# Kernel optimization log

Measured on AMD Instinct MI355X. Metric: run time of the kernel, lower is better.

The kernel has to match this reference:

```python
import jax, jax.numpy as jnp
import numpy as np

VOCAB, EDIM, ENC, H, OUT = 50000, 128, 128, 100, 104
B, L, NPT = 128, 64, 64          # batch, statements per seq, nodes per statement tree
N = B * L * NPT                  # 524288 total nodes
MAXD = 6                         # max depth of a 64-node complete binary tree


def setup_inputs() -> dict:
    key = jax.random.key(0)
    ks = jax.random.split(key, 14)
    tokens = jax.random.randint(ks[0], (N,), 0, VOCAB)
    # structured tree topology: each statement tree is a 64-node complete binary tree
    local = np.arange(NPT)
    par_local = np.where(local == 0, 0, (local - 1) // 2)
    depth_local = np.floor(np.log2(local + 1)).astype(np.int32)
    base = np.repeat(np.arange(B * L) * NPT, NPT)
    parent = jnp.asarray(base + np.tile(par_local, B * L), dtype=jnp.int32)
    depth = jnp.asarray(np.tile(depth_local, B * L), dtype=jnp.int32)
    tree_id = jnp.asarray(np.repeat(np.arange(B * L), NPT), dtype=jnp.int32)
    nrm = lambda k, s, sc: jax.random.normal(k, s, jnp.float32) * sc
    return {
        "tokens": tokens, "parent": parent, "depth": depth, "tree_id": tree_id,
        "emb": nrm(ks[1], (VOCAB, EDIM), 0.02),
        "W_lin": nrm(ks[2], (ENC, EDIM), 0.05), "b_lin": nrm(ks[3], (ENC,), 0.05),
        "Wi_f": nrm(ks[4], (3 * H, ENC), 0.05), "Wh_f": nrm(ks[5], (3 * H, H), 0.05),
        "bi_f": nrm(ks[6], (3 * H,), 0.05), "bh_f": nrm(ks[7], (3 * H,), 0.05),
        "Wi_b": nrm(ks[8], (3 * H, ENC), 0.05), "Wh_b": nrm(ks[9], (3 * H, H), 0.05),
        "bi_b": nrm(ks[10], (3 * H,), 0.05), "bh_b": nrm(ks[11], (3 * H,), 0.05),
        "W_fc": nrm(ks[12], (OUT, 2 * H), 0.05), "b_fc": nrm(ks[13], (OUT,), 0.05),
    }


def _gru_scan(x_seq, Wi, Wh, bi, bh):
    # x_seq: [L, B, ENC] -> outputs [L, B, H]. Matches torch.nn.GRU cell math.
    def step(hprev, xt):
        gi = xt @ Wi.T + bi              # [B, 3H]
        gh = hprev @ Wh.T + bh
        ir, iz, inn = jnp.split(gi, 3, axis=-1)
        hr, hz, hn = jnp.split(gh, 3, axis=-1)
        r = jax.nn.sigmoid(ir + hr)
        z = jax.nn.sigmoid(iz + hz)
        n = jnp.tanh(inn + r * hn)
        hnew = (1.0 - z) * n + z * hprev
        return hnew, hnew
    h0 = jnp.zeros((x_seq.shape[1], Wh.shape[1]), x_seq.dtype)
    _, ys = jax.lax.scan(step, h0, x_seq)
    return ys


def reference(tokens, parent, depth, tree_id, emb, W_lin, b_lin,
              Wi_f, Wh_f, bi_f, bh_f, Wi_b, Wh_b, bi_b, bh_b, W_fc, b_fc):
    # per-node value: linear(embedding(token))   [N, ENC]
    h = emb[tokens] @ W_lin.T + b_lin
    # bottom-up subtree sum: h(node) = v(node) + sum(h(children)), batched by depth level
    for d in range(MAXD, 0, -1):
        contrib = jnp.where((depth == d)[:, None], h, 0.0)
        h = h.at[parent].add(contrib)
    # TreeEncoder output: max over all node hidden states of each tree
    encodes = jax.ops.segment_max(h, tree_id, num_segments=B * L)  # [B*L, ENC]
    x = encodes.reshape(B, L, ENC).transpose(1, 0, 2)              # [L, B, ENC]
    yf = _gru_scan(x, Wi_f, Wh_f, bi_f, bh_f)                      # [L, B, H]
    yb = _gru_scan(x[::-1], Wi_b, Wh_b, bi_b, bh_b)[::-1]
    gru_out = jnp.concatenate([yf, yb], axis=-1)                   # [L, B, 2H]
    pooled = gru_out.max(axis=0)                                   # [B, 2H]
    return pooled @ W_fc.T + b_fc                                  # [B, OUT]
```

## Files before the change

kernel.cpp:

```cpp
#include <hip/hip_runtime.h>
#include <hip/hip_bf16.h>

typedef __bf16 bf16_t;
typedef __attribute__((ext_vector_type(8))) __bf16 bf16x8;
typedef __attribute__((ext_vector_type(4))) float f32x4;

#define TREES 8192
#define ENC 128
#define HH 100
#define G3 300
#define GSTRIDE 304
#define BB 128
#define LL 64
#define OUTD 104
#define TPB_TREES 8

__device__ __forceinline__ float sigm(float x) { return 1.0f / (1.0f + __expf(-x)); }
__device__ __forceinline__ float tanh_f(float x) { return 2.0f / (1.0f + __expf(-2.0f * x)) - 1.0f; }
__device__ __forceinline__ float bflo(unsigned int u) { return __builtin_bit_cast(float, u << 16); }
__device__ __forceinline__ float bfhi(unsigned int u) { return __builtin_bit_cast(float, u & 0xffff0000u); }

__device__ __forceinline__ void ldsbar() {
  asm volatile("s_waitcnt lgkmcnt(0)\n\ts_barrier" ::: "memory");
}

__device__ __forceinline__ int subtree_size(int n) {
  int np1 = n + 1;
  int d = 31 - __clz(np1);
  return ((64 >> d) - 1) + (((np1 & (np1 - 1)) == 0) ? 1 : 0);
}

__global__ __launch_bounds__(256) void k0_prep(const float* __restrict__ W_lin,
                                               const float* __restrict__ Wi_f,
                                               const float* __restrict__ Wi_b,
                                               const float* __restrict__ emb,
                                               bf16_t* __restrict__ Wbf,
                                               bf16_t* __restrict__ Wibf,
                                               bf16_t* __restrict__ embbf) {
  int i = blockIdx.x * 256 + threadIdx.x;
#pragma unroll
  for (int r = 0; r < 4; ++r) {
    int e = i + r * 524288;
    if (e < 1600000) {
      float4 v = ((const float4*)emb)[e];
      ushort4 u;
      u.x = __builtin_bit_cast(unsigned short, (bf16_t)v.x);
      u.y = __builtin_bit_cast(unsigned short, (bf16_t)v.y);
      u.z = __builtin_bit_cast(unsigned short, (bf16_t)v.z);
      u.w = __builtin_bit_cast(unsigned short, (bf16_t)v.w);
      ((ushort4*)embbf)[e] = u;
    }
  }
  if (i < 128 * 128) Wbf[i] = (bf16_t)W_lin[i];
  if (i < 608 * 128) {
    int jg = i >> 7, k = i & 127;
    int dir = (jg >= GSTRIDE) ? 1 : 0;
    int j = jg - dir * GSTRIDE;
    float v = 0.0f;
    if (j < G3) v = dir ? Wi_b[j * 128 + k] : Wi_f[j * 128 + k];
    Wibf[i] = (bf16_t)v;
  }
}

__global__ __launch_bounds__(256) void k1_tree(const int* __restrict__ tokens,
                                               const bf16_t* __restrict__ embbf,
                                               const bf16_t* __restrict__ Wbf,
                                               const float* __restrict__ b_lin,
                                               float* __restrict__ encodes) {
  __shared__ float s_[64][129];
  __shared__ float maxbuf[2][128];
  __shared__ float sb[128];
  int tid = threadIdx.x;
  int wave = tid >> 6;
  int lane = tid & 63;
  int ri = lane & 15;
  int kg = lane >> 4;
  int wm = wave >> 1;
  int wn = wave & 1;

  if (tid < 128) sb[tid] = b_lin[tid];

  bf16x8 bfr[4][4];
#pragma unroll
  for (int ks = 0; ks < 4; ++ks)
#pragma unroll
    for (int ni = 0; ni < 4; ++ni)
      bfr[ks][ni] = *(const bf16x8*)(Wbf + (size_t)((wn * 4 + ni) * 16 + ri) * 128 +
                                     ks * 32 + kg * 8);

  float szs[2][4];
#pragma unroll
  for (int mi = 0; mi < 2; ++mi)
#pragma unroll
    for (int rr = 0; rr < 4; ++rr)
      szs[mi][rr] = (float)subtree_size(wm * 32 + mi * 16 + kg * 4 + rr);

  int n = tid >> 2;
  int q = tid & 3;
  int c = tid >> 1;
  int half = tid & 1;
  int pc = (c & ~31) | ((((c >> 3) + (c >> 5)) & 3) << 3) | (c & 7);
  int tree0 = blockIdx.x * TPB_TREES;

  uint4 pre[4];
  {
    int tok = tokens[tree0 * 64 + n];
    const uint4* src = (const uint4*)(embbf + (size_t)tok * ENC) + q * 4;
#pragma unroll
    for (int i = 0; i < 4; ++i) pre[i] = src[i];
  }
  __syncthreads();

  for (int t = 0; t < TPB_TREES; ++t) {
    int tree = tree0 + t;

#pragma unroll
    for (int i = 0; i < 4; ++i) {
      uint4 p = pre[i];
      float4 f0 = {bflo(p.x), bfhi(p.x), bflo(p.y), bfhi(p.y)};
      float4 f1 = {bflo(p.z), bfhi(p.z), bflo(p.w), bfhi(p.w)};
      int col = q * 32 + (((i + q) & 3) << 3);
      *(float4*)&s_[n][col] = f0;
      *(float4*)&s_[n][col + 4] = f1;
    }

    if (t + 1 < TPB_TREES) {
      int tok = tokens[(tree + 1) * 64 + n];
      const uint4* src = (const uint4*)(embbf + (size_t)tok * ENC) + q * 4;
#pragma unroll
      for (int i = 0; i < 4; ++i) pre[i] = src[i];
    }
    ldsbar();

    if (half == 0) s_[31][pc] += s_[63][pc];
    {
      float r[8];
      int pb = 15 + half * 8;
#pragma unroll
      for (int i = 0; i < 8; ++i) {
        int p = pb + i;
        r[i] = s_[p][pc] + s_[2 * p + 1][pc] + s_[2 * p + 2][pc];
        s_[p][pc] = r[i];
      }
      float tt[4];
      int pb2 = 7 + half * 4;
#pragma unroll
      for (int i = 0; i < 4; ++i) {
        int p = pb2 + i;
        tt[i] = s_[p][pc] + r[2 * i] + r[2 * i + 1];
        s_[p][pc] = tt[i];
      }
      float uu[2];
      int pb3 = 3 + half * 2;
#pragma unroll
      for (int i = 0; i < 2; ++i) {
        int p = pb3 + i;
        uu[i] = s_[p][pc] + tt[2 * i] + tt[2 * i + 1];
        s_[p][pc] = uu[i];
      }
      int p1 = 1 + half;
      float w1 = s_[p1][pc] + uu[0] + uu[1];
      s_[p1][pc] = w1;
      float w2 = __shfl_xor(w1, 1);
      if (half == 0) s_[0][pc] = s_[0][pc] + w1 + w2;
    }
    ldsbar();

    f32x4 acc[2][4];
#pragma unroll
    for (int mi = 0; mi < 2; ++mi)
#pragma unroll
      for (int ni = 0; ni < 4; ++ni) {
        f32x4 z = {0.f, 0.f, 0.f, 0.f};
        acc[mi][ni] = z;
      }
#pragma unroll
    for (int ks = 0; ks < 4; ++ks) {
      int k0p = ks * 32 + (((kg + ks) & 3) << 3);
#pragma unroll
      for (int mi = 0; mi < 2; ++mi) {
        int row = wm * 32 + mi * 16 + ri;
        float4 a0 = *(const float4*)&s_[row][k0p];
        float4 a1 = *(const float4*)&s_[row][k0p + 4];
        bf16x8 afr;
        afr[0] = (bf16_t)a0.x; afr[1] = (bf16_t)a0.y; afr[2] = (bf16_t)a0.z; afr[3] = (bf16_t)a0.w;
        afr[4] = (bf16_t)a1.x; afr[5] = (bf16_t)a1.y; afr[6] = (bf16_t)a1.z; afr[7] = (bf16_t)a1.w;
#pragma unroll
        for (int ni = 0; ni < 4; ++ni)
          acc[mi][ni] = __builtin_amdgcn_mfma_f32_16x16x32_bf16(afr, bfr[ks][ni], acc[mi][ni], 0, 0, 0);
      }
    }

    float cmax[4];
#pragma unroll
    for (int ni = 0; ni < 4; ++ni) {
      float bl = sb[(wn * 4 + ni) * 16 + ri];
      float m = -1e30f;
#pragma unroll
      for (int mi = 0; mi < 2; ++mi) {
        f32x4 a = acc[mi][ni];
        m = fmaxf(m, fmaxf(fmaxf(a.x + szs[mi][0] * bl, a.y + szs[mi][1] * bl),
                           fmaxf(a.z + szs[mi][2] * bl, a.w + szs[mi][3] * bl)));
      }
      cmax[ni] = m;
    }
#pragma unroll
    for (int off = 16; off < 64; off <<= 1) {
#pragma unroll
      for (int ni = 0; ni < 4; ++ni)
        cmax[ni] = fmaxf(cmax[ni], __shfl_xor(cmax[ni], off));
    }
    if (lane < 16) {
#pragma unroll
      for (int ni = 0; ni < 4; ++ni) maxbuf[wm][(wn * 4 + ni) * 16 + lane] = cmax[ni];
    }
    ldsbar();
    if (tid < 128) {
      encodes[(size_t)tree * ENC + tid] = fmaxf(maxbuf[0][tid], maxbuf[1][tid]);
    }
  }
}

__global__ __launch_bounds__(256) void k2_gi(const float* __restrict__ encodes,
                                             const bf16_t* __restrict__ Wibf,
                                             const float* __restrict__ bi_f,
                                             const float* __restrict__ bi_b,
                                             bf16_t* __restrict__ GIb) {
  int tid = threadIdx.x;
  int wave = tid >> 6;
  int lane = tid & 63;
  int ri = lane & 15;
  int kg = lane >> 4;
  int m0 = blockIdx.x * 16;

  f32x4 acc[10];
#pragma unroll
  for (int i = 0; i < 10; ++i) {
    f32x4 z = {0.f, 0.f, 0.f, 0.f};
    acc[i] = z;
  }

  int r = m0 + ri;
  int er = (r & 127) * 64 + (r >> 7);
  const float* arow = encodes + (size_t)er * ENC;
#pragma unroll
  for (int ks = 0; ks < 4; ++ks) {
    int k0 = ks * 32 + kg * 8;
    float4 a0 = *(const float4*)(arow + k0);
    float4 a1 = *(const float4*)(arow + k0 + 4);
    bf16x8 afr;
    afr[0] = (bf16_t)a0.x; afr[1] = (bf16_t)a0.y; afr[2] = (bf16_t)a0.z; afr[3] = (bf16_t)a0.w;
    afr[4] = (bf16_t)a1.x; afr[5] = (bf16_t)a1.y; afr[6] = (bf16_t)a1.z; afr[7] = (bf16_t)a1.w;
#pragma unroll
    for (int i = 0; i < 10; ++i) {
      int nt = wave + i * 4;
      if (nt < 38) {
        bf16x8 bfr = *(const bf16x8*)(Wibf + (nt * 16 + ri) * 128 + k0);
        acc[i] = __builtin_amdgcn_mfma_f32_16x16x32_bf16(afr, bfr, acc[i], 0, 0, 0);
      }
    }
  }
#pragma unroll
  for (int i = 0; i < 10; ++i) {
    int nt = wave + i * 4;
    if (nt >= 38) continue;
    int jg = nt * 16 + ri;
    int dir = (jg >= GSTRIDE) ? 1 : 0;
    int j = jg - dir * GSTRIDE;
    if (j >= G3) continue;
    float bias = dir ? bi_b[j] : bi_f[j];
#pragma unroll
    for (int rr = 0; rr < 4; ++rr) {
      int rowg = m0 + kg * 4 + rr;
      int l = rowg >> 7, b = rowg & 127;
      GIb[(((size_t)dir * LL + l) * BB + b) * GSTRIDE + j] = (bf16_t)(acc[i][rr] + bias);
    }
  }
}

__global__ __launch_bounds__(640) void k3_gru(const bf16_t* __restrict__ GIb,
                                              const float* __restrict__ Wh_f,
                                              const float* __restrict__ Wh_b,
                                              const float* __restrict__ bh_f,
                                              const float* __restrict__ bh_b,
                                              float* __restrict__ pooled) {
  int blk = blockIdx.x;
  int dir = blk >> 7;
  int b = blk & 127;
  int tid = threadIdx.x;
  __shared__ __align__(16) float h_lds[104];
  __shared__ float gh_lds[304];
  __shared__ float gi_lds[2][304];
  const float* Wh = dir ? Wh_b : Wh_f;
  const float* bh = dir ? bh_b : bh_f;

  int j = tid >> 1;
  int kg = tid & 1;
  int kbase = kg * 52;
  bool isdot = (tid < 600);

  float4 wv[13];
  float bhj = 0.f;
  if (isdot) {
#pragma unroll
    for (int c = 0; c < 13; ++c) {
      int k0 = kbase + c * 4;
      float4 v;
      v.x = (k0 + 0 < HH) ? Wh[j * HH + k0 + 0] : 0.f;
      v.y = (k0 + 1 < HH) ? Wh[j * HH + k0 + 1] : 0.f;
      v.z = (k0 + 2 < HH) ? Wh[j * HH + k0 + 2] : 0.f;
      v.w = (k0 + 3 < HH) ? Wh[j * HH + k0 + 3] : 0.f;
      wv[c] = v;
    }
    if (kg == 0) bhj = bh[j];
  }
  if (tid < 104) h_lds[tid] = 0.f;

  const bf16_t* giB = GIb + (size_t)dir * LL * BB * GSTRIDE + (size_t)b * GSTRIDE;
  if (tid < G3) {
    int la0 = dir ? 63 : 0;
    gi_lds[0][tid] = (float)giB[(size_t)la0 * BB * GSTRIDE + tid];
  }
  float ymax = -1e30f;
  __syncthreads();

  for (int step = 0; step < 64; ++step) {
    int cur = step & 1;
    int nxt = cur ^ 1;
    float ginext = 0.f;
    if (tid < G3) {
      int ns = (step < 63) ? step + 1 : 63;
      int la = dir ? (63 - ns) : ns;
      ginext = (float)giB[(size_t)la * BB * GSTRIDE + tid];
    }
    if (isdot) {
      float a0 = 0.f, a1 = 0.f, a2 = 0.f, a3 = 0.f;
#pragma unroll
      for (int c = 0; c < 13; ++c) {
        float4 hv = *(const float4*)&h_lds[kbase + c * 4];
        a0 += wv[c].x * hv.x;
        a1 += wv[c].y * hv.y;
        a2 += wv[c].z * hv.z;
        a3 += wv[c].w * hv.w;
      }
      float p = (a0 + a1) + (a2 + a3);
      p += __shfl_xor(p, 1);
      if (kg == 0) gh_lds[j] = p + bhj;
    }
    __syncthreads();
    if (tid < HH) {
      float r = sigm(gi_lds[cur][tid] + gh_lds[tid]);
      float z = sigm(gi_lds[cur][100 + tid] + gh_lds[100 + tid]);
      float n = tanh_f(gi_lds[cur][200 + tid] + r * gh_lds[200 + tid]);
      float hnew = (1.f - z) * n + z * h_lds[tid];
      ymax = fmaxf(ymax, hnew);
      h_lds[tid] = hnew;
    }
    if (tid < G3 && step < 63) gi_lds[nxt][tid] = ginext;
    __syncthreads();
  }
  if (tid < HH) pooled[(size_t)b * 200 + dir * 100 + tid] = ymax;
}

__global__ __launch_bounds__(128) void k4_fc(const float* __restrict__ pooled,
                                             const float* __restrict__ W_fc,
                                             const float* __restrict__ b_fc,
                                             float* __restrict__ out) {
  int b = blockIdx.x;
  int o = threadIdx.x;
  if (o >= OUTD) return;
  const float* p = pooled + (size_t)b * 200;
  const float* w = W_fc + (size_t)o * 200;
  float acc = b_fc[o];
#pragma unroll 8
  for (int j = 0; j < 200; ++j) acc += p[j] * w[j];
  out[(size_t)b * OUTD + o] = acc;
}

extern "C" void kernel_launch(void* const* d_in, const int* in_sizes, int n_in,
                              void* d_out, int out_size, void* d_ws, size_t ws_size,
                              hipStream_t stream) {
  const int* tokens = (const int*)d_in[0];
  const float* emb = (const float*)d_in[4];
  const float* W_lin = (const float*)d_in[5];
  const float* b_lin = (const float*)d_in[6];
  const float* Wi_f = (const float*)d_in[7];
  const float* Wh_f = (const float*)d_in[8];
  const float* bi_f = (const float*)d_in[9];
  const float* bh_f = (const float*)d_in[10];
  const float* Wi_b = (const float*)d_in[11];
  const float* Wh_b = (const float*)d_in[12];
  const float* bi_b = (const float*)d_in[13];
  const float* bh_b = (const float*)d_in[14];
  const float* W_fc = (const float*)d_in[15];
  const float* b_fc = (const float*)d_in[16];

  float* encodes = (float*)d_ws;
  float* GIreg = encodes + (size_t)TREES * ENC;
  float* pooled = GIreg + (size_t)2 * LL * BB * GSTRIDE;
  bf16_t* Wbf = (bf16_t*)(pooled + (size_t)BB * 200);
  bf16_t* Wibf = Wbf + 128 * 128;
  bf16_t* embbf = (bf16_t*)GIreg;
  bf16_t* GIb = (bf16_t*)GIreg;

  k0_prep<<<2048, 256, 0, stream>>>(W_lin, Wi_f, Wi_b, emb, Wbf, Wibf, embbf);
  k1_tree<<<TREES / TPB_TREES, 256, 0, stream>>>(tokens, embbf, Wbf, b_lin, encodes);
  k2_gi<<<512, 256, 0, stream>>>(encodes, Wibf, bi_f, bi_b, GIb);
  k3_gru<<<256, 640, 0, stream>>>(GIb, Wh_f, Wh_b, bh_f, bh_b, pooled);
  k4_fc<<<BB, 128, 0, stream>>>(pooled, W_fc, b_fc, (float*)d_out);
}
```

Before: 152.5 us.

## Restructure GRU step to one barrier per step using shuffle-based gate exchange

The GRU recurrence kernel now assigns each hidden unit j an 8-lane group. Six lanes compute the r/z/n recurrent dot-product halves and exchange the partial sums through lane shuffles instead of an LDS gh buffer, so each step needs a single barrier instead of two. The hidden state is double-buffered in LDS, and the input-gate values are prefetched into registers instead of staged in LDS. The block grows from 640 to 832 threads, and two of every eight lanes sit idle. Weight rows are loaded as float4 with a zeroed tail.

```diff
diff --git a/kernel.cpp b/kernel.cpp
--- a/kernel.cpp
+++ b/kernel.cpp
@@ -278,7 +278,7 @@
   }
 }
 
-__global__ __launch_bounds__(640) void k3_gru(const bf16_t* __restrict__ GIb,
+__global__ __launch_bounds__(832) void k3_gru(const bf16_t* __restrict__ GIb,
                                               const float* __restrict__ Wh_f,
                                               const float* __restrict__ Wh_b,
                                               const float* __restrict__ bh_f,
@@ -288,78 +288,77 @@
   int dir = blk >> 7;
   int b = blk & 127;
   int tid = threadIdx.x;
-  __shared__ __align__(16) float h_lds[104];
-  __shared__ float gh_lds[304];
-  __shared__ float gi_lds[2][304];
+  __shared__ __align__(16) float h_lds[2][104];
+  int j = tid >> 3;
+  int sub = tid & 7;
+  int g = sub >> 1;
+  int half = sub & 1;
+  bool isdot = (sub < 6) && (j < HH);
+  bool isgate = (sub == 0) && (j < HH);
   const float* Wh = dir ? Wh_b : Wh_f;
   const float* bh = dir ? bh_b : bh_f;
 
-  int j = tid >> 1;
-  int kg = tid & 1;
-  int kbase = kg * 52;
-  bool isdot = (tid < 600);
-
   float4 wv[13];
-  float bhj = 0.f;
   if (isdot) {
-#pragma unroll
-    for (int c = 0; c < 13; ++c) {
-      int k0 = kbase + c * 4;
-      float4 v;
-      v.x = (k0 + 0 < HH) ? Wh[j * HH + k0 + 0] : 0.f;
-      v.y = (k0 + 1 < HH) ? Wh[j * HH + k0 + 1] : 0.f;
-      v.z = (k0 + 2 < HH) ? Wh[j * HH + k0 + 2] : 0.f;
-      v.w = (k0 + 3 < HH) ? Wh[j * HH + k0 + 3] : 0.f;
-      wv[c] = v;
-    }
-    if (kg == 0) bhj = bh[j];
-  }
-  if (tid < 104) h_lds[tid] = 0.f;
-
-  const bf16_t* giB = GIb + (size_t)dir * LL * BB * GSTRIDE + (size_t)b * GSTRIDE;
-  if (tid < G3) {
+    const float4* wrow = (const float4*)(Wh + (size_t)(g * HH + j) * HH + half * 52);
+#pragma unroll
+    for (int c = 0; c < 13; ++c) wv[c] = wrow[c];
+    if (half) { float4 z = {0.f, 0.f, 0.f, 0.f}; wv[12] = z; }
+  }
+  if (tid < 104) { h_lds[0][tid] = 0.f; h_lds[1][tid] = 0.f; }
+
+  float bhr = 0.f, bhz = 0.f, bhn = 0.f;
+  float gir = 0.f, giz = 0.f, gin = 0.f;
+  const bf16_t* gbase = nullptr;
+  if (isgate) {
+    bhr = bh[j]; bhz = bh[HH + j]; bhn = bh[2 * HH + j];
+    gbase = GIb + (size_t)dir * LL * BB * GSTRIDE + (size_t)b * GSTRIDE + j;
     int la0 = dir ? 63 : 0;
-    gi_lds[0][tid] = (float)giB[(size_t)la0 * BB * GSTRIDE + tid];
-  }
-  float ymax = -1e30f;
+    const bf16_t* p0 = gbase + (size_t)la0 * BB * GSTRIDE;
+    gir = (float)p0[0]; giz = (float)p0[100]; gin = (float)p0[200];
+  }
+  float h_prev = 0.f, ymax = -1e30f;
   __syncthreads();
 
+  int cur = 0;
   for (int step = 0; step < 64; ++step) {
-    int cur = step & 1;
-    int nxt = cur ^ 1;
-    float ginext = 0.f;
-    if (tid < G3) {
-      int ns = (step < 63) ? step + 1 : 63;
-      int la = dir ? (63 - ns) : ns;
-      ginext = (float)giB[(size_t)la * BB * GSTRIDE + tid];
-    }
+    float gnr = 0.f, gnz = 0.f, gnn = 0.f;
+    if (isgate && step < 63) {
+      int la = dir ? (62 - step) : (step + 1);
+      const bf16_t* p = gbase + (size_t)la * BB * GSTRIDE;
+      gnr = (float)p[0]; gnz = (float)p[100]; gnn = (float)p[200];
+    }
+    float p = 0.f;
     if (isdot) {
       float a0 = 0.f, a1 = 0.f, a2 = 0.f, a3 = 0.f;
+      const float* hb = &h_lds[cur][half * 52];
 #pragma unroll
       for (int c = 0; c < 13; ++c) {
-        float4 hv = *(const float4*)&h_lds[kbase + c * 4];
+        float4 hv = *(const float4*)(hb + c * 4);
         a0 += wv[c].x * hv.x;
         a1 += wv[c].y * hv.y;
         a2 += wv[c].z * hv.z;
         a3 += wv[c].w * hv.w;
       }
-      float p = (a0 + a1) + (a2 + a3);
-      p += __shfl_xor(p, 1);
-      if (kg == 0) gh_lds[j] = p + bhj;
-    }
-    __syncthreads();
-    if (tid < HH) {
-      float r = sigm(gi_lds[cur][tid] + gh_lds[tid]);
-      float z = sigm(gi_lds[cur][100 + tid] + gh_lds[100 + tid]);
-      float n = tanh_f(gi_lds[cur][200 + tid] + r * gh_lds[200 + tid]);
-      float hnew = (1.f - z) * n + z * h_lds[tid];
+      p = (a0 + a1) + (a2 + a3);
+    }
+    p += __shfl_xor(p, 1);
+    float gh2 = __shfl_xor(p, 2);
+    float gh4 = __shfl_xor(p, 4);
+    if (isgate) {
+      float r = sigm(gir + p + bhr);
+      float z = sigm(giz + gh2 + bhz);
+      float n = tanh_f(gin + r * (gh4 + bhn));
+      float hnew = (1.f - z) * n + z * h_prev;
       ymax = fmaxf(ymax, hnew);
-      h_lds[tid] = hnew;
-    }
-    if (tid < G3 && step < 63) gi_lds[nxt][tid] = ginext;
-    __syncthreads();
-  }
-  if (tid < HH) pooled[(size_t)b * 200 + dir * 100 + tid] = ymax;
+      h_lds[cur ^ 1][j] = hnew;
+      h_prev = hnew;
+      gir = gnr; giz = gnz; gin = gnn;
+    }
+    ldsbar();
+    cur ^= 1;
+  }
+  if (isgate) pooled[(size_t)b * 200 + dir * HH + j] = ymax;
 }
 
 __global__ __launch_bounds__(128) void k4_fc(const float* __restrict__ pooled,
@@ -406,6 +405,6 @@
   k0_prep<<<2048, 256, 0, stream>>>(W_lin, Wi_f, Wi_b, emb, Wbf, Wibf, embbf);
   k1_tree<<<TREES / TPB_TREES, 256, 0, stream>>>(tokens, embbf, Wbf, b_lin, encodes);
   k2_gi<<<512, 256, 0, stream>>>(encodes, Wibf, bi_f, bi_b, GIb);
-  k3_gru<<<256, 640, 0, stream>>>(GIb, Wh_f, Wh_b, bh_f, bh_b, pooled);
+  k3_gru<<<256, 832, 0, stream>>>(GIb, Wh_f, Wh_b, bh_f, bh_b, pooled);
   k4_fc<<<BB, 128, 0, stream>>>(pooled, W_fc, b_fc, (float*)d_out);
 }
```

New measurement: 187.4 us. 22.9% more time.

## Restructure GRU recurrent matvec to four rows per thread with half the threads

Applied to the files above, without the earlier changes.

The recurrent GRU kernel now runs 320 threads instead of 640. Each thread computes four gate rows over a quarter of the hidden dimension, so every h value read from LDS is reused across four rows, and the partial sums are combined with two xor shuffles. The recurrent biases move into the gate-update threads, and __syncthreads is replaced by an explicit lgkmcnt wait plus barrier. The aim is fewer LDS reads and fewer waves per barrier in this serial, latency-bound loop, at the cost of about 112 weight registers per thread.

```diff
diff --git a/kernel.cpp b/kernel.cpp
--- a/kernel.cpp
+++ b/kernel.cpp
@@ -278,7 +278,7 @@
   }
 }
 
-__global__ __launch_bounds__(640) void k3_gru(const bf16_t* __restrict__ GIb,
+__global__ __launch_bounds__(320) void k3_gru(const bf16_t* __restrict__ GIb,
                                               const float* __restrict__ Wh_f,
                                               const float* __restrict__ Wh_b,
                                               const float* __restrict__ bh_f,
@@ -288,33 +288,39 @@
   int dir = blk >> 7;
   int b = blk & 127;
   int tid = threadIdx.x;
-  __shared__ __align__(16) float h_lds[104];
+  __shared__ __align__(16) float h_lds[112];
   __shared__ float gh_lds[304];
   __shared__ float gi_lds[2][304];
   const float* Wh = dir ? Wh_b : Wh_f;
   const float* bh = dir ? bh_b : bh_f;
 
-  int j = tid >> 1;
-  int kg = tid & 1;
-  int kbase = kg * 52;
-  bool isdot = (tid < 600);
-
-  float4 wv[13];
-  float bhj = 0.f;
-  if (isdot) {
-#pragma unroll
-    for (int c = 0; c < 13; ++c) {
-      int k0 = kbase + c * 4;
-      float4 v;
-      v.x = (k0 + 0 < HH) ? Wh[j * HH + k0 + 0] : 0.f;
-      v.y = (k0 + 1 < HH) ? Wh[j * HH + k0 + 1] : 0.f;
-      v.z = (k0 + 2 < HH) ? Wh[j * HH + k0 + 2] : 0.f;
-      v.w = (k0 + 3 < HH) ? Wh[j * HH + k0 + 3] : 0.f;
-      wv[c] = v;
-    }
-    if (kg == 0) bhj = bh[j];
-  }
-  if (tid < 104) h_lds[tid] = 0.f;
+  int jg = tid >> 2;
+  int ksub = tid & 3;
+  bool isdot = (jg < 75);
+  int koff = (ksub == 0) ? 0 : (4 + ksub * 24);
+  int kn = (ksub == 0) ? 28 : 24;
+
+  float4 wv[4][7];
+#pragma unroll
+  for (int r = 0; r < 4; ++r)
+#pragma unroll
+    for (int c7 = 0; c7 < 7; ++c7) {
+      float4 v = {0.f, 0.f, 0.f, 0.f};
+      if (isdot) {
+        const float* wrow = Wh + (size_t)(jg * 4 + r) * HH + koff;
+        int c0 = c7 * 4;
+        if (c0 + 0 < kn) v.x = wrow[c0 + 0];
+        if (c0 + 1 < kn) v.y = wrow[c0 + 1];
+        if (c0 + 2 < kn) v.z = wrow[c0 + 2];
+        if (c0 + 3 < kn) v.w = wrow[c0 + 3];
+      }
+      wv[r][c7] = v;
+    }
+
+  if (tid < 112) h_lds[tid] = 0.f;
+
+  float bhr = 0.f, bhz = 0.f, bhn = 0.f;
+  if (tid < HH) { bhr = bh[tid]; bhz = bh[HH + tid]; bhn = bh[2 * HH + tid]; }
 
   const bf16_t* giB = GIb + (size_t)dir * LL * BB * GSTRIDE + (size_t)b * GSTRIDE;
   if (tid < G3) {
@@ -324,42 +330,56 @@
   float ymax = -1e30f;
   __syncthreads();
 
+  int cur = 0;
   for (int step = 0; step < 64; ++step) {
-    int cur = step & 1;
     int nxt = cur ^ 1;
     float ginext = 0.f;
-    if (tid < G3) {
-      int ns = (step < 63) ? step + 1 : 63;
-      int la = dir ? (63 - ns) : ns;
+    if (tid < G3 && step < 63) {
+      int la = dir ? (62 - step) : (step + 1);
       ginext = (float)giB[(size_t)la * BB * GSTRIDE + tid];
     }
+    f32x4 facc = {0.f, 0.f, 0.f, 0.f};
     if (isdot) {
+      float4 hv[7];
+#pragma unroll
+      for (int c7 = 0; c7 < 7; ++c7) hv[c7] = *(const float4*)&h_lds[koff + c7 * 4];
       float a0 = 0.f, a1 = 0.f, a2 = 0.f, a3 = 0.f;
 #pragma unroll
-      for (int c = 0; c < 13; ++c) {
-        float4 hv = *(const float4*)&h_lds[kbase + c * 4];
-        a0 += wv[c].x * hv.x;
-        a1 += wv[c].y * hv.y;
-        a2 += wv[c].z * hv.z;
-        a3 += wv[c].w * hv.w;
-      }
-      float p = (a0 + a1) + (a2 + a3);
-      p += __shfl_xor(p, 1);
-      if (kg == 0) gh_lds[j] = p + bhj;
-    }
-    __syncthreads();
+      for (int c7 = 0; c7 < 7; ++c7) {
+        a0 += wv[0][c7].x * hv[c7].x + wv[0][c7].y * hv[c7].y +
+              wv[0][c7].z * hv[c7].z + wv[0][c7].w * hv[c7].w;
+        a1 += wv[1][c7].x * hv[c7].x + wv[1][c7].y * hv[c7].y +
+              wv[1][c7].z * hv[c7].z + wv[1][c7].w * hv[c7].w;
+        a2 += wv[2][c7].x * hv[c7].x + wv[2][c7].y * hv[c7].y +
+              wv[2][c7].z * hv[c7].z + wv[2][c7].w * hv[c7].w;
+        a3 += wv[3][c7].x * hv[c7].x + wv[3][c7].y * hv[c7].y +
+              wv[3][c7].z * hv[c7].z + wv[3][c7].w * hv[c7].w;
+      }
+      facc[0] = a0; facc[1] = a1; facc[2] = a2; facc[3] = a3;
+    }
+#pragma unroll
+    for (int e = 0; e < 4; ++e) facc[e] += __shfl_xor(facc[e], 1);
+#pragma unroll
+    for (int e = 0; e < 4; ++e) facc[e] += __shfl_xor(facc[e], 2);
+    if (isdot) {
+      float out = (ksub == 0) ? facc[0] : (ksub == 1) ? facc[1]
+                : (ksub == 2) ? facc[2] : facc[3];
+      gh_lds[jg * 4 + ksub] = out;
+    }
+    ldsbar();
     if (tid < HH) {
-      float r = sigm(gi_lds[cur][tid] + gh_lds[tid]);
-      float z = sigm(gi_lds[cur][100 + tid] + gh_lds[100 + tid]);
-      float n = tanh_f(gi_lds[cur][200 + tid] + r * gh_lds[200 + tid]);
+      float r = sigm(gi_lds[cur][tid] + gh_lds[tid] + bhr);
+      float z = sigm(gi_lds[cur][100 + tid] + gh_lds[100 + tid] + bhz);
+      float n = tanh_f(gi_lds[cur][200 + tid] + r * (gh_lds[200 + tid] + bhn));
       float hnew = (1.f - z) * n + z * h_lds[tid];
       ymax = fmaxf(ymax, hnew);
       h_lds[tid] = hnew;
     }
     if (tid < G3 && step < 63) gi_lds[nxt][tid] = ginext;
-    __syncthreads();
-  }
-  if (tid < HH) pooled[(size_t)b * 200 + dir * 100 + tid] = ymax;
+    ldsbar();
+    cur = nxt;
+  }
+  if (tid < HH) pooled[(size_t)b * 200 + dir * HH + tid] = ymax;
 }
 
 __global__ __launch_bounds__(128) void k4_fc(const float* __restrict__ pooled,
@@ -406,6 +426,6 @@
   k0_prep<<<2048, 256, 0, stream>>>(W_lin, Wi_f, Wi_b, emb, Wbf, Wibf, embbf);
   k1_tree<<<TREES / TPB_TREES, 256, 0, stream>>>(tokens, embbf, Wbf, b_lin, encodes);
   k2_gi<<<512, 256, 0, stream>>>(encodes, Wibf, bi_f, bi_b, GIb);
-  k3_gru<<<256, 640, 0, stream>>>(GIb, Wh_f, Wh_b, bh_f, bh_b, pooled);
+  k3_gru<<<256, 320, 0, stream>>>(GIb, Wh_f, Wh_b, bh_f, bh_b, pooled);
   k4_fc<<<BB, 128, 0, stream>>>(pooled, W_fc, b_fc, (float*)d_out);
 }
```

Result: slower. 178.4 us (+17.0%).
